# Kernel optimization log

Measured on AMD Instinct MI355X. Metric: run time of the kernel, lower is better.

The kernel has to match this reference:

```python
import jax, jax.numpy as jnp
import numpy as np

B, T, D, H = 2, 2048, 1024, 16
DK = D // H  # 64


def setup_inputs() -> dict:
    key = jax.random.key(0)
    ks = jax.random.split(key, 13)
    s = 1.0 / np.sqrt(D)
    return {
        "x": jax.random.normal(ks[0], (B, T, D), jnp.float32),
        "Wq_w": jax.random.normal(ks[1], (D, D), jnp.float32) * s,
        "Wq_b": jax.random.normal(ks[2], (D,), jnp.float32) * 0.01,
        "Wk_w": jax.random.normal(ks[3], (D, D), jnp.float32) * s,
        "Wk_b": jax.random.normal(ks[4], (D,), jnp.float32) * 0.01,
        "Wv_w": jax.random.normal(ks[5], (D, D), jnp.float32) * s,
        "Wv_b": jax.random.normal(ks[6], (D,), jnp.float32) * 0.01,
        "Wo_w": jax.random.normal(ks[7], (D, D), jnp.float32) * s,
        "Wo_b": jax.random.normal(ks[8], (D,), jnp.float32) * 0.01,
        "qr": jax.random.normal(ks[9], (B, H, T, DK), jnp.float32),
        "qi": jax.random.normal(ks[10], (B, H, T, DK), jnp.float32),
        "kr": jax.random.normal(ks[11], (B, H, T, DK), jnp.float32),
        "ki": jax.random.normal(ks[12], (B, H, T, DK), jnp.float32),
    }


def _heads(y):
    # [B,T,D] -> [B,H,T,DK]
    return y.reshape(B, T, H, DK).transpose(0, 2, 1, 3)


def reference(x, Wq_w, Wq_b, Wk_w, Wk_b, Wv_w, Wv_b, Wo_w, Wo_b, qr, qi, kr, ki):
    Q = _heads(x @ Wq_w.T + Wq_b)
    K = _heads(x @ Wk_w.T + Wk_b)
    V = _heads(x @ Wv_w.T + Wv_b)
    # quantum noise: sin(atan2(imag, real))
    Q = Q + jnp.sin(jnp.arctan2(qi, qr))
    K = K + jnp.sin(jnp.arctan2(ki, kr))
    # Recursive fractal attention collapses: branches are identical and
    # deterministic, so (A1+A2)/2 == depth-0 attention at every level.
    scores = jnp.einsum("bhtd,bhsd->bhts", Q, K) / np.sqrt(DK).astype(np.float32)
    weights = jax.nn.softmax(scores, axis=-1)
    attn = jnp.einsum("bhts,bhsd->bhtd", weights, V)  # [B,H,T,DK]
    out = attn.transpose(0, 2, 1, 3).reshape(B, T, D)
    return out @ Wo_w.T + Wo_b
```

## Files before the change

kernel.cpp:

```cpp
#include <hip/hip_runtime.h>
#include <hip/hip_fp16.h>
#include <stdint.h>

typedef _Float16 half_t;
typedef _Float16 hf2 __attribute__((ext_vector_type(2)));
typedef _Float16 hf4 __attribute__((ext_vector_type(4)));
typedef _Float16 hf8 __attribute__((ext_vector_type(8)));
typedef float f32x16 __attribute__((ext_vector_type(16)));
typedef unsigned uint2_t __attribute__((ext_vector_type(2)));

#define LOG2E 1.4426950408889634f

__device__ __forceinline__ void gload16(const void* g, void* l) {
  __builtin_amdgcn_global_load_lds(
      (const __attribute__((address_space(1))) unsigned int*)g,
      (__attribute__((address_space(3))) unsigned int*)l, 16, 0, 0);
}

__device__ __forceinline__ unsigned packrtz(float a, float b) {
  auto h = __builtin_amdgcn_cvt_pkrtz(a, b);
  union { decltype(h) h2; unsigned u; } c;
  c.h2 = h;
  return c.u;
}

__device__ __forceinline__ float exp2fast(float x) {
#if __has_builtin(__builtin_amdgcn_exp2f)
  return __builtin_amdgcn_exp2f(x);
#else
  return exp2f(x);
#endif
}

__device__ __forceinline__ float psum2(unsigned pw, hf2 ones, float acc) {
#if __has_builtin(__builtin_amdgcn_fdot2)
  union { unsigned u; hf2 h; } c;
  c.u = pw;
  return __builtin_amdgcn_fdot2(c.h, ones, acc, false);
#else
  union { unsigned u; hf2 h; } c;
  c.u = pw;
  return acc + (float)c.h[0] + (float)c.h[1];
#endif
}

__global__ __launch_bounds__(256) void cvt_kernel(
    const float* __restrict__ x, const float* __restrict__ wq,
    const float* __restrict__ wk, const float* __restrict__ wv,
    const float* __restrict__ wo, half_t* __restrict__ xh,
    half_t* __restrict__ wh) {
  long e = ((long)blockIdx.x * 256 + threadIdx.x) * 16;
  const float* src;
  half_t* dst;
  if (e < 4194304L) {
    src = x + e;
    dst = xh + e;
  } else {
    long j = e - 4194304L;
    int w = (int)(j >> 20);
    long off = j & 1048575L;
    src = (w == 0 ? wq : w == 1 ? wk : w == 2 ? wv : wo) + off;
    dst = wh + ((long)w << 20) + off;
  }
  const float4* s4 = (const float4*)src;
  float4 f0 = s4[0], f1 = s4[1], f2 = s4[2], f3 = s4[3];
  hf8 o0 = {(half_t)f0.x, (half_t)f0.y, (half_t)f0.z, (half_t)f0.w,
            (half_t)f1.x, (half_t)f1.y, (half_t)f1.z, (half_t)f1.w};
  hf8 o1 = {(half_t)f2.x, (half_t)f2.y, (half_t)f2.z, (half_t)f2.w,
            (half_t)f3.x, (half_t)f3.y, (half_t)f3.z, (half_t)f3.w};
  *(hf8*)dst = o0;
  *(hf8*)(dst + 8) = o1;
}

__device__ __forceinline__ void gemm_core(const half_t* __restrict__ A,
                                          const half_t* __restrict__ Bt,
                                          int m0, int n0, half_t* lds,
                                          f32x16 acc[2][2]) {
  const int tid = threadIdx.x;
  const int wid = tid >> 6;
  const int lane = tid & 63;
  const int l31 = lane & 31;
  const int hh = lane >> 5;
  const int wm = wid >> 1, wn = wid & 1;
  char* ldsb = (char*)lds;

#pragma unroll
  for (int mt = 0; mt < 2; mt++)
#pragma unroll
    for (int nt = 0; nt < 2; nt++)
#pragma unroll
      for (int i = 0; i < 16; i++) acc[mt][nt][i] = 0.f;

  int goA[4], goB[4];
#pragma unroll
  for (int i = 0; i < 4; i++) {
    int c = i * 256 + tid;
    int row = c >> 3;
    int c16 = (c & 7) ^ (row & 7);
    goA[i] = (m0 + row) * 1024 + c16 * 8;
    goB[i] = (n0 + row) * 1024 + c16 * 8;
  }
  int aof[4], bof[4];
#pragma unroll
  for (int kc = 0; kc < 4; kc++) {
    int swz = (kc * 32 + hh * 16) ^ ((l31 & 7) << 4);
    aof[kc] = (wm * 64 + l31) * 128 + swz;
    bof[kc] = 16384 + (wn * 64 + l31) * 128 + swz;
  }

  for (int kt = 0; kt < 16; ++kt) {
#pragma unroll
    for (int i = 0; i < 4; i++) {
      gload16(A + goA[i], ldsb + i * 4096 + wid * 1024);
      gload16(Bt + goB[i], ldsb + 16384 + i * 4096 + wid * 1024);
      goA[i] += 64;
      goB[i] += 64;
    }
    __syncthreads();
#pragma unroll
    for (int kc = 0; kc < 4; kc++) {
      hf8 af[2], bf[2];
#pragma unroll
      for (int mt = 0; mt < 2; mt++)
        af[mt] = *(const hf8*)(ldsb + aof[kc] + mt * 4096);
#pragma unroll
      for (int nt = 0; nt < 2; nt++)
        bf[nt] = *(const hf8*)(ldsb + bof[kc] + nt * 4096);
#pragma unroll
      for (int mt = 0; mt < 2; mt++)
#pragma unroll
        for (int nt = 0; nt < 2; nt++)
          acc[mt][nt] = __builtin_amdgcn_mfma_f32_32x32x16_f16(
              af[mt], bf[nt], acc[mt][nt], 0, 0, 0);
    }
    __syncthreads();
  }
}

__global__ __launch_bounds__(256, 2) void proj_kernel(
    const half_t* __restrict__ xh, const half_t* __restrict__ wh,
    const float* __restrict__ bq, const float* __restrict__ bk,
    const float* __restrict__ bv, const float* __restrict__ qr,
    const float* __restrict__ qi, const float* __restrict__ kr,
    const float* __restrict__ ki, half_t* __restrict__ Qh,
    half_t* __restrict__ Kh, half_t* __restrict__ Vth) {
  __shared__ __align__(16) half_t lds[16384];
  const int z = blockIdx.z;
  const half_t* Bt = wh + (size_t)z * 1048576;
  const int m0 = blockIdx.x * 128, n0 = blockIdx.y * 128;
  f32x16 acc[2][2];
  gemm_core(xh, Bt, m0, n0, lds, acc);

  const int tid = threadIdx.x;
  const int wid = tid >> 6;
  const int lane = tid & 63;
  const int l31 = lane & 31;
  const int hh = lane >> 5;
  const int wm = wid >> 1, wn = wid & 1;
  const float* bias = (z == 0) ? bq : (z == 1) ? bk : bv;
  const float* nr = (z == 0) ? qr : kr;
  const float* ni = (z == 0) ? qi : ki;
  const float scale = (z == 0) ? (0.125f * LOG2E) : 1.0f;

#pragma unroll
  for (int nt = 0; nt < 2; nt++) {
    const int n = n0 + wn * 64 + nt * 32 + l31;
    const float bsv = bias[n];
    const int hd = n >> 6, d = n & 63;
#pragma unroll
    for (int mt = 0; mt < 2; mt++) {
      const int mbase = m0 + wm * 64 + mt * 32;
      if (z == 2) {
#pragma unroll
        for (int g = 0; g < 4; g++) {
          const int m = mbase + 8 * g + 4 * hh;
          const int bb = m >> 11, tt = m & 2047;
          hf4 pk;
#pragma unroll
          for (int i2 = 0; i2 < 4; i2++)
            pk[i2] = (half_t)(acc[mt][nt][4 * g + i2] + bsv);
          *(hf4*)(Vth + (((size_t)(bb * 16 + hd) * 64 + d) * 2048 + tt)) = pk;
        }
      } else {
        half_t* dstp = (z == 0) ? Qh : Kh;
#pragma unroll
        for (int r = 0; r < 16; r++) {
          const int m = mbase + (r & 3) + 8 * (r >> 2) + 4 * hh;
          const int bb = m >> 11, tt = m & 2047;
          const size_t idx = ((size_t)(bb * 16 + hd) * 2048 + tt) * 64 + d;
          float v = acc[mt][nt][r] + bsv;
          const float a_ = nr[idx], b_ = ni[idx];
          v += b_ * rsqrtf(a_ * a_ + b_ * b_);
          dstp[idx] = (half_t)(v * scale);
        }
      }
    }
  }
}

template <int CUR>
__device__ __forceinline__ void attn_tile_t(
    bool stage, const half_t* __restrict__ Kb, const half_t* __restrict__ Vb,
    char* base, int qw, int& gk0, int& gk1, int& gv0, int& gv1,
    const int kofs[4], const hf8 qf[4], const f32x16& zv, f32x16 ot[2],
    float& psAcc, hf2 ones) {
  if (stage) {
    gload16(Kb + gk0, base + (CUR ^ 1) * 8192 + qw * 1024);
    gload16(Kb + gk1, base + (CUR ^ 1) * 8192 + 4096 + qw * 1024);
    gload16(Vb + gv0, base + 16384 + (CUR ^ 1) * 8192 + qw * 1024);
    gload16(Vb + gv1, base + 16384 + (CUR ^ 1) * 8192 + 4096 + qw * 1024);
    gk0 += 4096;
    gk1 += 4096;
    gv0 += 64;
    gv1 += 64;
  }
#pragma unroll
  for (int kt = 0; kt < 2; kt++) {
    __builtin_amdgcn_s_setprio(1);
    f32x16 s = __builtin_amdgcn_mfma_f32_32x32x16_f16(
        *(const hf8*)(base + kofs[0] + CUR * 8192 + kt * 4096), qf[0], zv, 0, 0,
        0);
    s = __builtin_amdgcn_mfma_f32_32x32x16_f16(
        *(const hf8*)(base + kofs[1] + CUR * 8192 + kt * 4096), qf[1], s, 0, 0,
        0);
    s = __builtin_amdgcn_mfma_f32_32x32x16_f16(
        *(const hf8*)(base + kofs[2] + CUR * 8192 + kt * 4096), qf[2], s, 0, 0,
        0);
    s = __builtin_amdgcn_mfma_f32_32x32x16_f16(
        *(const hf8*)(base + kofs[3] + CUR * 8192 + kt * 4096), qf[3], s, 0, 0,
        0);
    __builtin_amdgcn_s_setprio(0);

    unsigned pw[8];
#pragma unroll
    for (int j = 0; j < 8; j++) {
      float p0 = exp2fast(s[2 * j]);
      float p1 = exp2fast(s[2 * j + 1]);
      pw[j] = packrtz(p0, p1);
      psAcc = psum2(pw[j], ones, psAcc);
    }

#pragma unroll
    for (int sub = 0; sub < 2; sub++) {
      const int kc = kt * 2 + sub;
      unsigned a0 = pw[sub * 4 + 0], a1 = pw[sub * 4 + 1];
      unsigned a2 = pw[sub * 4 + 2], a3 = pw[sub * 4 + 3];
      union { unsigned u[4]; hf8 v; } pu;
#if __has_builtin(__builtin_amdgcn_permlane32_swap)
      uint2_t r02 = __builtin_amdgcn_permlane32_swap(a0, a2, false, false);
      uint2_t r13 = __builtin_amdgcn_permlane32_swap(a1, a3, false, false);
      pu.u[0] = r02[0];
      pu.u[1] = r13[0];
      pu.u[2] = r02[1];
      pu.u[3] = r13[1];
#else
      const int hh_ = (threadIdx.x & 63) >> 5;
      unsigned x0 = __shfl_xor(a0, 32, 64), x1 = __shfl_xor(a1, 32, 64);
      unsigned x2 = __shfl_xor(a2, 32, 64), x3 = __shfl_xor(a3, 32, 64);
      pu.u[0] = hh_ ? x2 : a0;
      pu.u[1] = hh_ ? x3 : a1;
      pu.u[2] = hh_ ? a2 : x0;
      pu.u[3] = hh_ ? a3 : x1;
#endif
      __builtin_amdgcn_s_setprio(1);
#pragma unroll
      for (int dt = 0; dt < 2; dt++) {
        hf8 vf =
            *(const hf8*)(base + kofs[kc] + 16384 + CUR * 8192 + dt * 4096);
        ot[dt] =
            __builtin_amdgcn_mfma_f32_32x32x16_f16(vf, pu.v, ot[dt], 0, 0, 0);
      }
      __builtin_amdgcn_s_setprio(0);
    }
  }
  __syncthreads();
}

__global__ __launch_bounds__(512, 4) void attn_kernel(
    const half_t* __restrict__ Qh, const half_t* __restrict__ Kh,
    const half_t* __restrict__ Vth, half_t* __restrict__ ah) {
  __shared__ __align__(16) char smem[65536];
  const int tid = threadIdx.x, wid = tid >> 6, lane = tid & 63;
  const int l31 = lane & 31, hh = lane >> 5;
  const int qw = wid & 3, g = wid >> 2;
  const int lin = blockIdx.x;
  const int slot = lin >> 3;
  const int bh = (lin & 7) * 4 + (slot >> 4);
  const int qb = slot & 15;
  const int b = bh >> 4, hd = bh & 15;
  const int t = qb * 128 + qw * 32 + l31;

  char* base = smem + g * 32768;

  const half_t* qrow = Qh + ((size_t)bh * 2048 + t) * 64;
  hf8 qf[4];
#pragma unroll
  for (int kc = 0; kc < 4; kc++) qf[kc] = *(const hf8*)(qrow + kc * 16 + hh * 8);

  f32x16 ot[2];
#pragma unroll
  for (int dt = 0; dt < 2; dt++)
#pragma unroll
    for (int i = 0; i < 16; i++) ot[dt][i] = 0.f;
  f32x16 zv;
#pragma unroll
  for (int i = 0; i < 16; i++) zv[i] = 0.f;
  float psAcc = 0.f;
  const hf2 ones = {(_Float16)1.0f, (_Float16)1.0f};

  const half_t* Kb = Kh + (size_t)bh * 2048 * 64;
  const half_t* Vb = Vth + (size_t)bh * 64 * 2048;
  const int kvbase = g * 1024;

  int kofs[4];
#pragma unroll
  for (int kc = 0; kc < 4; kc++)
    kofs[kc] = l31 * 128 + ((kc * 32 + hh * 16) ^ ((l31 & 7) << 4));

  int gk0, gk1, gv0, gv1;
  {
    int c0 = qw * 64 + lane, c1 = 256 + qw * 64 + lane;
    int r0 = c0 >> 3, s0 = (c0 & 7) ^ (r0 & 7);
    int r1 = c1 >> 3, s1 = (c1 & 7) ^ (r1 & 7);
    gk0 = (kvbase + r0) * 64 + s0 * 8;
    gk1 = (kvbase + r1) * 64 + s1 * 8;
    gv0 = r0 * 2048 + kvbase + s0 * 8;
    gv1 = r1 * 2048 + kvbase + s1 * 8;
  }
  gload16(Kb + gk0, base + qw * 1024);
  gload16(Kb + gk1, base + 4096 + qw * 1024);
  gload16(Vb + gv0, base + 16384 + qw * 1024);
  gload16(Vb + gv1, base + 16384 + 4096 + qw * 1024);
  gk0 += 4096;
  gk1 += 4096;
  gv0 += 64;
  gv1 += 64;
  __syncthreads();

  for (int tp = 0; tp < 8; ++tp) {
    attn_tile_t<0>(true, Kb, Vb, base, qw, gk0, gk1, gv0, gv1, kofs, qf, zv,
                   ot, psAcc, ones);
    attn_tile_t<1>(tp < 7, Kb, Vb, base, qw, gk0, gk1, gv0, gv1, kofs, qf, zv,
                   ot, psAcc, ones);
  }

  const float lrun = psAcc + __shfl_xor(psAcc, 32, 64);

  float* cb = (float*)smem;
  float* lb = (float*)(smem + 32768);
  if (g == 1) {
#pragma unroll
    for (int dt = 0; dt < 2; dt++)
#pragma unroll
      for (int i = 0; i < 16; i++)
        cb[((qw * 2 + dt) * 16 + i) * 64 + lane] = ot[dt][i];
    lb[qw * 64 + lane] = lrun;
  }
  __syncthreads();
  if (g == 0) {
#pragma unroll
    for (int dt = 0; dt < 2; dt++)
#pragma unroll
      for (int i = 0; i < 16; i++)
        ot[dt][i] += cb[((qw * 2 + dt) * 16 + i) * 64 + lane];
    const float inv = 1.0f / (lrun + lb[qw * 64 + lane]);
    const size_t obase = ((size_t)b * 2048 + t) * 1024 + hd * 64;
#pragma unroll
    for (int dt = 0; dt < 2; dt++)
#pragma unroll
      for (int gg = 0; gg < 4; gg++) {
        hf4 pk;
#pragma unroll
        for (int i2 = 0; i2 < 4; i2++)
          pk[i2] = (half_t)(ot[dt][4 * gg + i2] * inv);
        *(hf4*)(ah + obase + dt * 32 + 8 * gg + 4 * hh) = pk;
      }
  }
}

__global__ __launch_bounds__(256, 2) void outproj_kernel(
    const half_t* __restrict__ ah, const half_t* __restrict__ woh,
    const float* __restrict__ bo, float* __restrict__ out) {
  __shared__ __align__(16) half_t lds[16384];
  const int m0 = blockIdx.x * 128, n0 = blockIdx.y * 128;
  f32x16 acc[2][2];
  gemm_core(ah, woh, m0, n0, lds, acc);
  const int tid = threadIdx.x, wid = tid >> 6, lane = tid & 63;
  const int l31 = lane & 31, hh = lane >> 5;
  const int wm = wid >> 1, wn = wid & 1;
#pragma unroll
  for (int nt = 0; nt < 2; nt++) {
    const int n = n0 + wn * 64 + nt * 32 + l31;
    const float bsv = bo[n];
#pragma unroll
    for (int mt = 0; mt < 2; mt++) {
      const int mbase = m0 + wm * 64 + mt * 32;
#pragma unroll
      for (int r = 0; r < 16; r++) {
        const int m = mbase + (r & 3) + 8 * (r >> 2) + 4 * hh;
        out[(size_t)m * 1024 + n] = acc[mt][nt][r] + bsv;
      }
    }
  }
}

extern "C" void kernel_launch(void* const* d_in, const int* in_sizes, int n_in,
                              void* d_out, int out_size, void* d_ws,
                              size_t ws_size, hipStream_t stream) {
  const float* x = (const float*)d_in[0];
  const float* Wq = (const float*)d_in[1];
  const float* bq = (const float*)d_in[2];
  const float* Wk = (const float*)d_in[3];
  const float* bk = (const float*)d_in[4];
  const float* Wv = (const float*)d_in[5];
  const float* bv = (const float*)d_in[6];
  const float* Wo = (const float*)d_in[7];
  const float* bo = (const float*)d_in[8];
  const float* qr = (const float*)d_in[9];
  const float* qi = (const float*)d_in[10];
  const float* kr = (const float*)d_in[11];
  const float* ki = (const float*)d_in[12];
  float* out = (float*)d_out;

  char* ws = (char*)d_ws;
  half_t* xh = (half_t*)(ws);
  half_t* wh = (half_t*)(ws + 8388608);
  half_t* Qh = (half_t*)(ws + 16777216);
  half_t* Kh = (half_t*)(ws + 25165824);
  half_t* Vth = (half_t*)(ws + 33554432);
  half_t* ah = (half_t*)(ws + 41943040);

  cvt_kernel<<<dim3(2048), dim3(256), 0, stream>>>(x, Wq, Wk, Wv, Wo, xh, wh);
  proj_kernel<<<dim3(32, 8, 3), dim3(256), 0, stream>>>(
      xh, wh, bq, bk, bv, qr, qi, kr, ki, Qh, Kh, Vth);
  attn_kernel<<<dim3(512), dim3(512), 0, stream>>>(Qh, Kh, Vth, ah);
  outproj_kernel<<<dim3(32, 8), dim3(256), 0, stream>>>(ah, wh + 3 * 1048576, bo,
                                                        out);
}
```

Measured before the change: 112.2 us.

## Double-buffer LDS in projection GEMMs to overlap global loads with MFMA

```diff
diff --git a/kernel.cpp b/kernel.cpp
--- a/kernel.cpp
+++ b/kernel.cpp
@@ -72,9 +72,47 @@
   *(hf8*)(dst + 8) = o1;
 }
 
+template <int CUR>
+__device__ __forceinline__ void gstep(bool stage, const half_t* __restrict__ A,
+                                      const half_t* __restrict__ Bt,
+                                      char* ldsb, int wid, int& goA, int& goB,
+                                      int aof0, int aof1, int aof2, int aof3,
+                                      int bof0, int bof1, int bof2, int bof3,
+                                      f32x16 acc[2][2]) {
+  if (stage) {
+#pragma unroll
+    for (int i = 0; i < 4; i++) {
+      gload16(A + goA + i * 32768,
+              ldsb + (CUR ^ 1) * 16384 + i * 4096 + wid * 1024);
+      gload16(Bt + goB + i * 32768,
+              ldsb + 32768 + (CUR ^ 1) * 16384 + i * 4096 + wid * 1024);
+    }
+    goA += 64;
+    goB += 64;
+  }
+#pragma unroll
+  for (int kc = 0; kc < 4; kc++) {
+    const int ao = (kc == 0 ? aof0 : kc == 1 ? aof1 : kc == 2 ? aof2 : aof3);
+    const int bo = (kc == 0 ? bof0 : kc == 1 ? bof1 : kc == 2 ? bof2 : bof3);
+    hf8 af0 = *(const hf8*)(ldsb + CUR * 16384 + ao);
+    hf8 af1 = *(const hf8*)(ldsb + CUR * 16384 + ao + 4096);
+    hf8 bf0 = *(const hf8*)(ldsb + 32768 + CUR * 16384 + bo);
+    hf8 bf1 = *(const hf8*)(ldsb + 32768 + CUR * 16384 + bo + 4096);
+    acc[0][0] =
+        __builtin_amdgcn_mfma_f32_32x32x16_f16(af0, bf0, acc[0][0], 0, 0, 0);
+    acc[0][1] =
+        __builtin_amdgcn_mfma_f32_32x32x16_f16(af0, bf1, acc[0][1], 0, 0, 0);
+    acc[1][0] =
+        __builtin_amdgcn_mfma_f32_32x32x16_f16(af1, bf0, acc[1][0], 0, 0, 0);
+    acc[1][1] =
+        __builtin_amdgcn_mfma_f32_32x32x16_f16(af1, bf1, acc[1][1], 0, 0, 0);
+  }
+  __syncthreads();
+}
+
 __device__ __forceinline__ void gemm_core(const half_t* __restrict__ A,
                                           const half_t* __restrict__ Bt,
-                                          int m0, int n0, half_t* lds,
+                                          int m0, int n0, char* ldsb,
                                           f32x16 acc[2][2]) {
   const int tid = threadIdx.x;
   const int wid = tid >> 6;
@@ -82,7 +120,6 @@
   const int l31 = lane & 31;
   const int hh = lane >> 5;
   const int wm = wid >> 1, wn = wid & 1;
-  char* ldsb = (char*)lds;
 
 #pragma unroll
   for (int mt = 0; mt < 2; mt++)
@@ -91,49 +128,36 @@
 #pragma unroll
       for (int i = 0; i < 16; i++) acc[mt][nt][i] = 0.f;
 
-  int goA[4], goB[4];
+  const int rowb = tid >> 3;
+  const int c16 = (tid & 7) ^ (rowb & 7);
+  int goA = (m0 + rowb) * 1024 + c16 * 8;
+  int goB = (n0 + rowb) * 1024 + c16 * 8;
+
+  const int swz0 = (hh * 16) ^ ((l31 & 7) << 4);
+  const int swz1 = (32 + hh * 16) ^ ((l31 & 7) << 4);
+  const int swz2 = (64 + hh * 16) ^ ((l31 & 7) << 4);
+  const int swz3 = (96 + hh * 16) ^ ((l31 & 7) << 4);
+  const int arow = (wm * 64 + l31) * 128;
+  const int brow = (wn * 64 + l31) * 128;
+  const int aof0 = arow + swz0, aof1 = arow + swz1, aof2 = arow + swz2,
+            aof3 = arow + swz3;
+  const int bof0 = brow + swz0, bof1 = brow + swz1, bof2 = brow + swz2,
+            bof3 = brow + swz3;
+
 #pragma unroll
   for (int i = 0; i < 4; i++) {
-    int c = i * 256 + tid;
-    int row = c >> 3;
-    int c16 = (c & 7) ^ (row & 7);
-    goA[i] = (m0 + row) * 1024 + c16 * 8;
-    goB[i] = (n0 + row) * 1024 + c16 * 8;
-  }
-  int aof[4], bof[4];
-#pragma unroll
-  for (int kc = 0; kc < 4; kc++) {
-    int swz = (kc * 32 + hh * 16) ^ ((l31 & 7) << 4);
-    aof[kc] = (wm * 64 + l31) * 128 + swz;
-    bof[kc] = 16384 + (wn * 64 + l31) * 128 + swz;
-  }
-
-  for (int kt = 0; kt < 16; ++kt) {
-#pragma unroll
-    for (int i = 0; i < 4; i++) {
-      gload16(A + goA[i], ldsb + i * 4096 + wid * 1024);
-      gload16(Bt + goB[i], ldsb + 16384 + i * 4096 + wid * 1024);
-      goA[i] += 64;
-      goB[i] += 64;
-    }
-    __syncthreads();
-#pragma unroll
-    for (int kc = 0; kc < 4; kc++) {
-      hf8 af[2], bf[2];
-#pragma unroll
-      for (int mt = 0; mt < 2; mt++)
-        af[mt] = *(const hf8*)(ldsb + aof[kc] + mt * 4096);
-#pragma unroll
-      for (int nt = 0; nt < 2; nt++)
-        bf[nt] = *(const hf8*)(ldsb + bof[kc] + nt * 4096);
-#pragma unroll
-      for (int mt = 0; mt < 2; mt++)
-#pragma unroll
-        for (int nt = 0; nt < 2; nt++)
-          acc[mt][nt] = __builtin_amdgcn_mfma_f32_32x32x16_f16(
-              af[mt], bf[nt], acc[mt][nt], 0, 0, 0);
-    }
-    __syncthreads();
+    gload16(A + goA + i * 32768, ldsb + i * 4096 + wid * 1024);
+    gload16(Bt + goB + i * 32768, ldsb + 32768 + i * 4096 + wid * 1024);
+  }
+  goA += 64;
+  goB += 64;
+  __syncthreads();
+
+  for (int kp = 0; kp < 8; ++kp) {
+    gstep<0>(true, A, Bt, ldsb, wid, goA, goB, aof0, aof1, aof2, aof3, bof0,
+             bof1, bof2, bof3, acc);
+    gstep<1>(kp < 7, A, Bt, ldsb, wid, goA, goB, aof0, aof1, aof2, aof3, bof0,
+             bof1, bof2, bof3, acc);
   }
 }
 
@@ -144,12 +168,12 @@
     const float* __restrict__ qi, const float* __restrict__ kr,
     const float* __restrict__ ki, half_t* __restrict__ Qh,
     half_t* __restrict__ Kh, half_t* __restrict__ Vth) {
-  __shared__ __align__(16) half_t lds[16384];
+  __shared__ __align__(16) char ldsb[65536];
   const int z = blockIdx.z;
   const half_t* Bt = wh + (size_t)z * 1048576;
   const int m0 = blockIdx.x * 128, n0 = blockIdx.y * 128;
   f32x16 acc[2][2];
-  gemm_core(xh, Bt, m0, n0, lds, acc);
+  gemm_core(xh, Bt, m0, n0, ldsb, acc);
 
   const int tid = threadIdx.x;
   const int wid = tid >> 6;
@@ -381,10 +405,10 @@
 __global__ __launch_bounds__(256, 2) void outproj_kernel(
     const half_t* __restrict__ ah, const half_t* __restrict__ woh,
     const float* __restrict__ bo, float* __restrict__ out) {
-  __shared__ __align__(16) half_t lds[16384];
+  __shared__ __align__(16) char ldsb[65536];
   const int m0 = blockIdx.x * 128, n0 = blockIdx.y * 128;
   f32x16 acc[2][2];
-  gemm_core(ah, woh, m0, n0, lds, acc);
+  gemm_core(ah, woh, m0, n0, ldsb, acc);
   const int tid = threadIdx.x, wid = tid >> 6, lane = tid & 63;
   const int l31 = lane & 31, hh = lane >> 5;
   const int wm = wid >> 1, wn = wid & 1;
```

New measurement: 110.8 us. Within noise of the previous version (-1.3%).
